# Kernel tuning notes

Measured on AMD Instinct MI355X. Metric: run time of the kernel, lower is better.

Reference implementation:

```python
import jax, jax.numpy as jnp
from jax import lax
import numpy as np

B = 262144
CLASSES = 11


def setup_inputs() -> dict:
    key = jax.random.key(0)
    ks = jax.random.split(key, 8)
    exponents = jax.random.randint(ks[0], (B, 16), 0, CLASSES, dtype=jnp.int32)
    conv0_w = jax.random.normal(ks[1], (4, 12, 1, 2), jnp.float32) * 0.1
    conv0_b = jax.random.normal(ks[2], (4,), jnp.float32) * 0.05
    conv1_w = jax.random.normal(ks[3], (4, 12, 2, 1), jnp.float32) * 0.1
    # xavier-uniform linears, bias filled with 0.01 (as in init_weights)
    lim1 = float(np.sqrt(6.0 / (96 + 256)))
    linear_w = jax.random.uniform(ks[4], (256, 96), jnp.float32, -lim1, lim1)
    linear_b = jnp.full((256,), 0.01, jnp.float32)
    lim2 = float(np.sqrt(6.0 / (256 + 4)))
    out_w = jax.random.uniform(ks[5], (4, 256), jnp.float32, -lim2, lim2)
    out_b = jnp.full((4,), 0.01, jnp.float32)
    return {"exponents": exponents, "conv0_w": conv0_w, "conv0_b": conv0_b,
            "conv1_w": conv1_w, "linear_w": linear_w, "linear_b": linear_b,
            "out_w": out_w, "out_b": out_b}


def _conv(x, w):
    return lax.conv_general_dilated(x, w, (1, 1), 'VALID',
                                    dimension_numbers=('NCHW', 'OIHW', 'NCHW'))


def _forward(exponents, conv0_w, conv0_b, conv1_w, linear_w, linear_b, out_w, out_b):
    e = exponents.reshape(-1, 4, 4)
    # reconstruct board values: 0 tile stays 0, else 2**e
    x = jnp.where(e == 0, 0.0, jnp.exp2(e.astype(jnp.float32)))  # [B,4,4]
    # rotate_normalize: flips chosen from argmax corner (computed BEFORE flipping)
    corners = jnp.stack([x[:, 0, 0], x[:, 0, -1], x[:, -1, 0], x[:, -1, -1]], axis=1)
    ix = jnp.argmax(corners, axis=1)
    flip_v = ix >= 2          # floor(ix/2) == 1
    flip_h = (ix % 2) == 1
    x = jnp.where(flip_v[:, None, None], x[:, ::-1, :], x)
    x = jnp.where(flip_h[:, None, None], x[:, :, ::-1], x)
    # log2 with 0 -> 0, one-hot over 11 classes
    x_log = jnp.log2(x + (x == 0).astype(jnp.float32))
    onehot = jax.nn.one_hot(jnp.round(x_log).astype(jnp.int32), CLASSES,
                            dtype=jnp.float32)          # [B,4,4,11]
    onehot = jnp.transpose(onehot, (0, 3, 1, 2))         # [B,11,4,4]
    mask = onehot.sum(axis=1, keepdims=True)             # channel 0 (all ones)
    feat = jnp.concatenate([mask, onehot], axis=1)       # [B,12,4,4]
    zh = jax.nn.relu(_conv(feat, conv0_w) + conv0_b[None, :, None, None])  # [B,4,4,3]
    zv = jax.nn.relu(_conv(feat, conv1_w))                                  # [B,4,3,4]
    z1 = jnp.concatenate([zh.reshape(-1, 48), zv.reshape(-1, 48)], axis=1)  # [B,96]
    z2 = jax.nn.relu(z1 @ linear_w.T + linear_b)                            # [B,256]
    probs = jax.nn.softmax(z2 @ out_w.T + out_b, axis=1)                    # [B,4]
    # unscramble: vert swaps actions (0,1); horiz swaps actions (2,3)
    perm = jnp.stack([jnp.where(flip_v, 1, 0), jnp.where(flip_v, 0, 1),
                      jnp.where(flip_h, 3, 2), jnp.where(flip_h, 2, 3)], axis=1)
    return jnp.take_along_axis(probs, perm, axis=1)


def reference(exponents, conv0_w, conv0_b, conv1_w, linear_w, linear_b, out_w, out_b):
    return _forward(exponents, conv0_w, conv0_b, conv1_w, linear_w, linear_b, out_w, out_b)
```

## Files before the change

kernel.cpp:

```cpp
#include <hip/hip_runtime.h>

typedef unsigned int  u32;
typedef unsigned short u16;

typedef float    f4  __attribute__((ext_vector_type(4)));
typedef short    bf8 __attribute__((ext_vector_type(8)));
typedef __fp16   h8  __attribute__((ext_vector_type(8)));
typedef __fp16   h2  __attribute__((ext_vector_type(2)));

#define NBLK  1024
#define ITERS 4
#define ZSTR  104

#define WS_AF   0
#define WS_OW   49152
#define WS_TAB  57344

__device__ __forceinline__ u32 bfr(float f) {
    union { float f; u32 u; } v; v.f = f;
    return (v.u + 0x8000u) >> 16;
}
__device__ __forceinline__ u32 pk2(float lo, float hi) { return bfr(lo) | (bfr(hi) << 16); }
__device__ __forceinline__ u32 pkh(float lo, float hi) {
    union { h2 h; u32 u; } v; v.h = __builtin_amdgcn_cvt_pkrtz(lo, hi); return v.u;
}
__device__ __forceinline__ u32 nrev(u32 x) {
    return ((x >> 12) & 0xFu) | ((x >> 4) & 0xF0u) | ((x << 4) & 0xF00u) | ((x << 12) & 0xF000u);
}

__launch_bounds__(256)
__global__ void smartcnn_prep(const float* __restrict__ c0w, const float* __restrict__ c0b,
                              const float* __restrict__ c1w,
                              const float* __restrict__ lw,  const float* __restrict__ ow,
                              u16* __restrict__ wsAf, u32* __restrict__ wsOw,
                              uint2* __restrict__ wsTab)
{
    const int i = blockIdx.x * 256 + threadIdx.x;
    if (i < 24576) {
        const int j    = i & 7;
        const int lane = (i >> 3) & 63;
        const int rest = i >> 9;
        const int m  = lane & 15, qd = lane >> 4;
        const int s  = rest % 3;
        const int wtt = rest / 3;
        const int tt = wtt & 3, w = wtt >> 2;
        const int tbase = ((tt & 1) ? 4 : 0) + ((tt >> 1) ? 32 : 0);
        const int fid = 64*w + tbase + 8*(m >> 2) + (m & 3);
        const int kp = s*32 + qd*8 + j;
        const int kq = (kp < 48) ? kp : kp - 48;
        const int ko = ((kp < 48) ? 0 : 48) + (kq & 3)*12 + (kq >> 2);
        wsAf[i] = (u16)bfr(lw[fid*96 + ko]);
    } else if (i < 26624) {
        const int t = i - 24576;
        const int k    = t & 3;
        const int lane = (t >> 2) & 63;
        const int wc   = t >> 8;
        const int m = lane & 15, qd = lane >> 4;
        const int c = wc & 1, w = wc >> 1;
        u32 val = 0u;
        if (m < 4) {
            const int n8 = 64*w + 32*c + qd*8;
            val = pkh(ow[m*256 + n8 + 2*k], ow[m*256 + n8 + 2*k + 1]);
        }
        wsOw[t] = val;
    } else if (i < 26866) {
        const int t = i - 26624;
        const int e = (t < 121) ? t : t - 121;
        const int v1 = e / 11, v2 = e - v1*11;
        float a[4];
        #pragma unroll
        for (int c = 0; c < 4; ++c) {
            if (t < 121)
                a[c] = fmaxf(c0w[c*24 + 0] + c0w[c*24 + (1+v1)*2 + 0] + c0b[c]
                           + c0w[c*24 + 1] + c0w[c*24 + (1+v2)*2 + 1], 0.f);
            else
                a[c] = fmaxf(c1w[c*24 + 0] + c1w[c*24 + (1+v1)*2 + 0]
                           + c1w[c*24 + 1] + c1w[c*24 + (1+v2)*2 + 1], 0.f);
        }
        wsTab[t] = make_uint2(pk2(a[0], a[1]), pk2(a[2], a[3]));
    }
}

__device__ __forceinline__ void phase1_fn(const int4 e4, u16* __restrict__ z1b, u32* __restrict__ flgb,
                                          const uint2* __restrict__ Th, const uint2* __restrict__ Tv,
                                          const int w, const int m, const int qd)
{
    u32 pkd = (u32)e4.x | ((u32)e4.y << 4) | ((u32)e4.z << 8) | ((u32)e4.w << 12);
    u32 R0 = (u32)__shfl((int)pkd, m);
    u32 R1 = (u32)__shfl((int)pkd, m + 16);
    u32 R2 = (u32)__shfl((int)pkd, m + 32);
    u32 R3 = (u32)__shfl((int)pkd, m + 48);
    u32 c0v = R0 & 15u, c1v = (R0 >> 12) & 15u, c2v = R3 & 15u, c3v = (R3 >> 12) & 15u;
    u32 best = c0v; int ix = 0;
    if (c1v > best) { best = c1v; ix = 1; }
    if (c2v > best) { best = c2v; ix = 2; }
    if (c3v > best) { best = c3v; ix = 3; }
    const bool fv = (ix >= 2), fh = ((ix & 1) != 0);
    u32 F[4];
    F[0] = fv ? R3 : R0;
    F[1] = fv ? R2 : R1;
    F[2] = fv ? R1 : R2;
    F[3] = fv ? R0 : R3;
    #pragma unroll
    for (int i = 0; i < 4; ++i) F[i] = fh ? nrev(F[i]) : F[i];

    if (qd == 0) flgb[w*16 + m] = (u32)fv | ((u32)fh << 1);

    const u32 Fq = F[qd];
    u32 nbq[4], nbc[4];
    #pragma unroll
    for (int j = 0; j < 4; ++j) nbq[j] = (Fq >> (4*j)) & 15u;
    #pragma unroll
    for (int i = 0; i < 4; ++i) nbc[i] = (F[i] >> (4*qd)) & 15u;

    uint2 H0 = Th[nbq[0]*11u + nbq[1]];
    uint2 H1 = Th[nbq[1]*11u + nbq[2]];
    uint2 H2 = Th[nbq[2]*11u + nbq[3]];
    uint2 V0 = Tv[nbc[0]*11u + nbc[1]];
    uint2 V1 = Tv[nbc[1]*11u + nbc[2]];
    uint2 V2 = Tv[nbc[2]*11u + nbc[3]];

    u16* zrow = &z1b[(w*16 + m) * ZSTR];
    *(uint2*)(zrow + (qd*3 + 0)*4) = H0;
    *(uint2*)(zrow + (qd*3 + 1)*4) = H1;
    *(uint2*)(zrow + (qd*3 + 2)*4) = H2;
    *(uint2*)(zrow + 48 + (0*4 + qd)*4) = V0;
    *(uint2*)(zrow + 48 + (1*4 + qd)*4) = V1;
    *(uint2*)(zrow + 48 + (2*4 + qd)*4) = V2;
}

__device__ __forceinline__ void gemm_fn(const u16* __restrict__ z1b, float4* __restrict__ Pb,
                                        const bf8 (&af)[4][3], const u32 (&owA)[2][4], const f4 (&lb4)[4],
                                        const int w, const int m, const int qd)
{
    #pragma unroll
    for (int G = 0; G < 4; ++G) {
        bf8 zb[3];
        #pragma unroll
        for (int s = 0; s < 3; ++s)
            zb[s] = *(const bf8*)(&z1b[(G*16 + m)*ZSTR + s*32 + qd*8]);

        f4 acc_t[4] = {lb4[0], lb4[1], lb4[2], lb4[3]};
        #pragma unroll
        for (int s = 0; s < 3; ++s)
            #pragma unroll
            for (int tt = 0; tt < 4; ++tt)
                acc_t[tt] = __builtin_amdgcn_mfma_f32_16x16x32_bf16(af[tt][s], zb[s], acc_t[tt], 0, 0, 0);

        f4 acc2 = {0.f, 0.f, 0.f, 0.f};
        #pragma unroll
        for (int c = 0; c < 2; ++c) {
            union { u32 u[4]; h8 v; } bu, au;
            bu.u[0] = pkh(fmaxf(acc_t[2*c  ][0], 0.f), fmaxf(acc_t[2*c  ][1], 0.f));
            bu.u[1] = pkh(fmaxf(acc_t[2*c  ][2], 0.f), fmaxf(acc_t[2*c  ][3], 0.f));
            bu.u[2] = pkh(fmaxf(acc_t[2*c+1][0], 0.f), fmaxf(acc_t[2*c+1][1], 0.f));
            bu.u[3] = pkh(fmaxf(acc_t[2*c+1][2], 0.f), fmaxf(acc_t[2*c+1][3], 0.f));
            au.u[0] = owA[c][0]; au.u[1] = owA[c][1]; au.u[2] = owA[c][2]; au.u[3] = owA[c][3];
            acc2 = __builtin_amdgcn_mfma_f32_16x16x32_f16(au.v, bu.v, acc2, 0, 0, 0);
        }
        if (qd == 0)
            Pb[(G*4 + w)*16 + m] = make_float4(acc2[0], acc2[1], acc2[2], acc2[3]);
    }
}

__device__ __forceinline__ void epi_fn(const float4* __restrict__ Pb, const u32 fl, const float4 obv,
                                       float* __restrict__ out, const int base, const int m, const int qd)
{
    float4 s0 = Pb[(qd*4 + 0)*16 + m], s1 = Pb[(qd*4 + 1)*16 + m];
    float4 s2 = Pb[(qd*4 + 2)*16 + m], s3 = Pb[(qd*4 + 3)*16 + m];
    float L0 = s0.x + s1.x + s2.x + s3.x + obv.x;
    float L1 = s0.y + s1.y + s2.y + s3.y + obv.y;
    float L2 = s0.z + s1.z + s2.z + s3.z + obv.z;
    float L3 = s0.w + s1.w + s2.w + s3.w + obv.w;
    float mx = fmaxf(fmaxf(L0, L1), fmaxf(L2, L3));
    float e0 = __expf(L0 - mx), e1 = __expf(L1 - mx), e2 = __expf(L2 - mx), e3 = __expf(L3 - mx);
    float inv = __builtin_amdgcn_rcpf(e0 + e1 + e2 + e3);
    float p0 = e0 * inv, p1 = e1 * inv, p2 = e2 * inv, p3 = e3 * inv;
    float4 o;
    o.x = (fl & 1u) ? p1 : p0;
    o.y = (fl & 1u) ? p0 : p1;
    o.z = (fl & 2u) ? p3 : p2;
    o.w = (fl & 2u) ? p2 : p3;
    *(float4*)(out + (size_t)(base + qd*16 + m) * 4) = o;
}

__launch_bounds__(256, 4)
__global__ void smartcnn_fused(const int* __restrict__ exps,
                               const float* __restrict__ lb, const float* __restrict__ ob,
                               const u16* __restrict__ wsAf, const u32* __restrict__ wsOw,
                               const uint2* __restrict__ wsTab,
                               float* __restrict__ out)
{
    __shared__ uint2  ThA[121];
    __shared__ uint2  TvA[121];
    __shared__ u16    z1A[64 * ZSTR];
    __shared__ u16    z1B[64 * ZSTR];
    __shared__ float4 PbA[4*4*16];
    __shared__ float4 PbB[4*4*16];
    __shared__ u32    flgA[64];
    __shared__ u32    flgB[64];

    const int tid  = threadIdx.x;
    const int w    = tid >> 6;
    const int lane = tid & 63;
    const int m    = lane & 15;
    const int qd   = lane >> 4;

    if (tid < 242) {
        uint2 v = wsTab[tid];
        if (tid < 121) ThA[tid] = v; else TvA[tid - 121] = v;
    }

    bf8 af[4][3];
    #pragma unroll
    for (int tt = 0; tt < 4; ++tt)
        #pragma unroll
        for (int s = 0; s < 3; ++s)
            af[tt][s] = *(const bf8*)(wsAf + (((w*4 + tt)*3 + s) << 9) + (lane << 3));

    u32 owA[2][4];
    #pragma unroll
    for (int c = 0; c < 2; ++c) {
        uint4 t = *(const uint4*)(wsOw + ((((w*2 + c) << 6) + lane) << 2));
        owA[c][0] = t.x; owA[c][1] = t.y; owA[c][2] = t.z; owA[c][3] = t.w;
    }

    f4 lb4[4];
    #pragma unroll
    for (int tt = 0; tt < 4; ++tt) {
        const int tbase = ((tt & 1) ? 4 : 0) + ((tt >> 1) ? 32 : 0);
        lb4[tt] = *(const f4*)(lb + 64*w + tbase + 8*qd);
    }
    const float4 obv = *(const float4*)ob;

    const int b0 = blockIdx.x * (ITERS * 64);
    __syncthreads();

    int4 e4 = *(const int4*)(exps + (size_t)(b0 + w*16 + m)*16 + qd*4);
    phase1_fn(e4, z1A, flgA, &ThA[0], &TvA[0], w, m, qd);
    e4 = *(const int4*)(exps + (size_t)(b0 + 64 + w*16 + m)*16 + qd*4);
    __syncthreads();

    #pragma unroll
    for (int itp = 0; itp < ITERS/2; ++itp) {
        const int it = itp * 2;

        const u32 flA = flgA[qd*16 + m];
        phase1_fn(e4, z1B, flgB, &ThA[0], &TvA[0], w, m, qd);
        if (it + 2 < ITERS)
            e4 = *(const int4*)(exps + (size_t)(b0 + (it+2)*64 + w*16 + m)*16 + qd*4);
        gemm_fn(z1A, PbA, af, owA, lb4, w, m, qd);

        __syncthreads();

        const u32 flB = flgB[qd*16 + m];
        if (it + 2 < ITERS) {
            phase1_fn(e4, z1A, flgA, &ThA[0], &TvA[0], w, m, qd);
            if (it + 3 < ITERS)
                e4 = *(const int4*)(exps + (size_t)(b0 + (it+3)*64 + w*16 + m)*16 + qd*4);
        }
        epi_fn(PbA, flA, obv, out, b0 + it*64, m, qd);
        gemm_fn(z1B, PbB, af, owA, lb4, w, m, qd);

        __syncthreads();

        epi_fn(PbB, flB, obv, out, b0 + (it+1)*64, m, qd);
    }
}

extern "C" void kernel_launch(void* const* d_in, const int* in_sizes, int n_in,
                              void* d_out, int out_size, void* d_ws, size_t ws_size,
                              hipStream_t stream) {
    const int*   exps = (const int*)  d_in[0];
    const float* c0w  = (const float*)d_in[1];
    const float* c0b  = (const float*)d_in[2];
    const float* c1w  = (const float*)d_in[3];
    const float* lw   = (const float*)d_in[4];
    const float* lbv  = (const float*)d_in[5];
    const float* oww  = (const float*)d_in[6];
    const float* obv  = (const float*)d_in[7];
    u16*   wsAf  = (u16*)  ((char*)d_ws + WS_AF);
    u32*   wsOw  = (u32*)  ((char*)d_ws + WS_OW);
    uint2* wsTab = (uint2*)((char*)d_ws + WS_TAB);
    smartcnn_prep<<<105, 256, 0, stream>>>(c0w, c0b, c1w, lw, oww, wsAf, wsOw, wsTab);
    smartcnn_fused<<<NBLK, 256, 0, stream>>>(exps, lbv, obv, wsAf, wsOw, wsTab, (float*)d_out);
}
```

Measured before the change: 93.64 us.

## Give each wave full hidden dimension to remove cross-wave reduction and barriers

Measured after the change: 175.7 us. 87.6% more time.

```diff
diff --git a/kernel.cpp b/kernel.cpp
--- a/kernel.cpp
+++ b/kernel.cpp
@@ -8,8 +8,8 @@
 typedef __fp16   h8  __attribute__((ext_vector_type(8)));
 typedef __fp16   h2  __attribute__((ext_vector_type(2)));
 
-#define NBLK  1024
-#define ITERS 4
+#define NBLK  512
+#define ITERS 8
 #define ZSTR  104
 
 #define WS_AF   0
@@ -23,6 +23,9 @@
 __device__ __forceinline__ u32 pk2(float lo, float hi) { return bfr(lo) | (bfr(hi) << 16); }
 __device__ __forceinline__ u32 pkh(float lo, float hi) {
     union { h2 h; u32 u; } v; v.h = __builtin_amdgcn_cvt_pkrtz(lo, hi); return v.u;
+}
+__device__ __forceinline__ u32 pkmax0(u32 x) {
+    u32 r; asm("v_pk_max_f16 %0, %1, %2" : "=v"(r) : "v"(x), "v"(0u)); return r;
 }
 __device__ __forceinline__ u32 nrev(u32 x) {
     return ((x >> 12) & 0xFu) | ((x >> 4) & 0xF0u) | ((x << 4) & 0xF00u) | ((x << 12) & 0xF000u);
@@ -81,124 +84,17 @@
     }
 }
 
-__device__ __forceinline__ void phase1_fn(const int4 e4, u16* __restrict__ z1b, u32* __restrict__ flgb,
-                                          const uint2* __restrict__ Th, const uint2* __restrict__ Tv,
-                                          const int w, const int m, const int qd)
-{
-    u32 pkd = (u32)e4.x | ((u32)e4.y << 4) | ((u32)e4.z << 8) | ((u32)e4.w << 12);
-    u32 R0 = (u32)__shfl((int)pkd, m);
-    u32 R1 = (u32)__shfl((int)pkd, m + 16);
-    u32 R2 = (u32)__shfl((int)pkd, m + 32);
-    u32 R3 = (u32)__shfl((int)pkd, m + 48);
-    u32 c0v = R0 & 15u, c1v = (R0 >> 12) & 15u, c2v = R3 & 15u, c3v = (R3 >> 12) & 15u;
-    u32 best = c0v; int ix = 0;
-    if (c1v > best) { best = c1v; ix = 1; }
-    if (c2v > best) { best = c2v; ix = 2; }
-    if (c3v > best) { best = c3v; ix = 3; }
-    const bool fv = (ix >= 2), fh = ((ix & 1) != 0);
-    u32 F[4];
-    F[0] = fv ? R3 : R0;
-    F[1] = fv ? R2 : R1;
-    F[2] = fv ? R1 : R2;
-    F[3] = fv ? R0 : R3;
-    #pragma unroll
-    for (int i = 0; i < 4; ++i) F[i] = fh ? nrev(F[i]) : F[i];
-
-    if (qd == 0) flgb[w*16 + m] = (u32)fv | ((u32)fh << 1);
-
-    const u32 Fq = F[qd];
-    u32 nbq[4], nbc[4];
-    #pragma unroll
-    for (int j = 0; j < 4; ++j) nbq[j] = (Fq >> (4*j)) & 15u;
-    #pragma unroll
-    for (int i = 0; i < 4; ++i) nbc[i] = (F[i] >> (4*qd)) & 15u;
-
-    uint2 H0 = Th[nbq[0]*11u + nbq[1]];
-    uint2 H1 = Th[nbq[1]*11u + nbq[2]];
-    uint2 H2 = Th[nbq[2]*11u + nbq[3]];
-    uint2 V0 = Tv[nbc[0]*11u + nbc[1]];
-    uint2 V1 = Tv[nbc[1]*11u + nbc[2]];
-    uint2 V2 = Tv[nbc[2]*11u + nbc[3]];
-
-    u16* zrow = &z1b[(w*16 + m) * ZSTR];
-    *(uint2*)(zrow + (qd*3 + 0)*4) = H0;
-    *(uint2*)(zrow + (qd*3 + 1)*4) = H1;
-    *(uint2*)(zrow + (qd*3 + 2)*4) = H2;
-    *(uint2*)(zrow + 48 + (0*4 + qd)*4) = V0;
-    *(uint2*)(zrow + 48 + (1*4 + qd)*4) = V1;
-    *(uint2*)(zrow + 48 + (2*4 + qd)*4) = V2;
-}
-
-__device__ __forceinline__ void gemm_fn(const u16* __restrict__ z1b, float4* __restrict__ Pb,
-                                        const bf8 (&af)[4][3], const u32 (&owA)[2][4], const f4 (&lb4)[4],
-                                        const int w, const int m, const int qd)
-{
-    #pragma unroll
-    for (int G = 0; G < 4; ++G) {
-        bf8 zb[3];
-        #pragma unroll
-        for (int s = 0; s < 3; ++s)
-            zb[s] = *(const bf8*)(&z1b[(G*16 + m)*ZSTR + s*32 + qd*8]);
-
-        f4 acc_t[4] = {lb4[0], lb4[1], lb4[2], lb4[3]};
-        #pragma unroll
-        for (int s = 0; s < 3; ++s)
-            #pragma unroll
-            for (int tt = 0; tt < 4; ++tt)
-                acc_t[tt] = __builtin_amdgcn_mfma_f32_16x16x32_bf16(af[tt][s], zb[s], acc_t[tt], 0, 0, 0);
-
-        f4 acc2 = {0.f, 0.f, 0.f, 0.f};
-        #pragma unroll
-        for (int c = 0; c < 2; ++c) {
-            union { u32 u[4]; h8 v; } bu, au;
-            bu.u[0] = pkh(fmaxf(acc_t[2*c  ][0], 0.f), fmaxf(acc_t[2*c  ][1], 0.f));
-            bu.u[1] = pkh(fmaxf(acc_t[2*c  ][2], 0.f), fmaxf(acc_t[2*c  ][3], 0.f));
-            bu.u[2] = pkh(fmaxf(acc_t[2*c+1][0], 0.f), fmaxf(acc_t[2*c+1][1], 0.f));
-            bu.u[3] = pkh(fmaxf(acc_t[2*c+1][2], 0.f), fmaxf(acc_t[2*c+1][3], 0.f));
-            au.u[0] = owA[c][0]; au.u[1] = owA[c][1]; au.u[2] = owA[c][2]; au.u[3] = owA[c][3];
-            acc2 = __builtin_amdgcn_mfma_f32_16x16x32_f16(au.v, bu.v, acc2, 0, 0, 0);
-        }
-        if (qd == 0)
-            Pb[(G*4 + w)*16 + m] = make_float4(acc2[0], acc2[1], acc2[2], acc2[3]);
-    }
-}
-
-__device__ __forceinline__ void epi_fn(const float4* __restrict__ Pb, const u32 fl, const float4 obv,
-                                       float* __restrict__ out, const int base, const int m, const int qd)
-{
-    float4 s0 = Pb[(qd*4 + 0)*16 + m], s1 = Pb[(qd*4 + 1)*16 + m];
-    float4 s2 = Pb[(qd*4 + 2)*16 + m], s3 = Pb[(qd*4 + 3)*16 + m];
-    float L0 = s0.x + s1.x + s2.x + s3.x + obv.x;
-    float L1 = s0.y + s1.y + s2.y + s3.y + obv.y;
-    float L2 = s0.z + s1.z + s2.z + s3.z + obv.z;
-    float L3 = s0.w + s1.w + s2.w + s3.w + obv.w;
-    float mx = fmaxf(fmaxf(L0, L1), fmaxf(L2, L3));
-    float e0 = __expf(L0 - mx), e1 = __expf(L1 - mx), e2 = __expf(L2 - mx), e3 = __expf(L3 - mx);
-    float inv = __builtin_amdgcn_rcpf(e0 + e1 + e2 + e3);
-    float p0 = e0 * inv, p1 = e1 * inv, p2 = e2 * inv, p3 = e3 * inv;
-    float4 o;
-    o.x = (fl & 1u) ? p1 : p0;
-    o.y = (fl & 1u) ? p0 : p1;
-    o.z = (fl & 2u) ? p3 : p2;
-    o.w = (fl & 2u) ? p2 : p3;
-    *(float4*)(out + (size_t)(base + qd*16 + m) * 4) = o;
-}
-
-__launch_bounds__(256, 4)
+__launch_bounds__(256, 2)
 __global__ void smartcnn_fused(const int* __restrict__ exps,
                                const float* __restrict__ lb, const float* __restrict__ ob,
                                const u16* __restrict__ wsAf, const u32* __restrict__ wsOw,
                                const uint2* __restrict__ wsTab,
                                float* __restrict__ out)
 {
-    __shared__ uint2  ThA[121];
-    __shared__ uint2  TvA[121];
-    __shared__ u16    z1A[64 * ZSTR];
-    __shared__ u16    z1B[64 * ZSTR];
-    __shared__ float4 PbA[4*4*16];
-    __shared__ float4 PbB[4*4*16];
-    __shared__ u32    flgA[64];
-    __shared__ u32    flgB[64];
+    __shared__ u16   afL[48 * 512];
+    __shared__ uint2 ThA[121];
+    __shared__ uint2 TvA[121];
+    __shared__ u16   z1[64 * ZSTR];
 
     const int tid  = threadIdx.x;
     const int w    = tid >> 6;
@@ -210,61 +106,126 @@
         uint2 v = wsTab[tid];
         if (tid < 121) ThA[tid] = v; else TvA[tid - 121] = v;
     }
-
-    bf8 af[4][3];
     #pragma unroll
-    for (int tt = 0; tt < 4; ++tt)
+    for (int f2 = 0; f2 < 12; ++f2) {
+        const int f = w * 12 + f2;
+        uint4 t = *(const uint4*)((const char*)wsAf + f * 1024 + lane * 16);
+        *(uint4*)((char*)afL + f * 1024 + lane * 16) = t;
+    }
+    u32 owA[8][4];
+    #pragma unroll
+    for (int c = 0; c < 8; ++c) {
+        uint4 t = *(const uint4*)(wsOw + c * 256 + lane * 4);
+        owA[c][0] = t.x; owA[c][1] = t.y; owA[c][2] = t.z; owA[c][3] = t.w;
+    }
+    f4 lbT[16];
+    #pragma unroll
+    for (int T = 0; T < 16; ++T) {
+        const int tbase = ((T & 1) ? 4 : 0) + ((T >> 1) * 32);
+        lbT[T] = *(const f4*)(lb + tbase + 8 * qd);
+    }
+    const float4 obv = *(const float4*)ob;
+
+    const int bb = blockIdx.x * (ITERS * 64);
+    __syncthreads();
+
+    int4 e4 = *(const int4*)(exps + (size_t)(bb + w*16 + m)*16 + qd*4);
+
+    #pragma unroll 1
+    for (int it = 0; it < ITERS; ++it) {
+        u32 pkd = (u32)e4.x | ((u32)e4.y << 4) | ((u32)e4.z << 8) | ((u32)e4.w << 12);
+        const int itn = (it + 1 < ITERS) ? it + 1 : it;
+        int4 e4n = *(const int4*)(exps + (size_t)(bb + itn*64 + w*16 + m)*16 + qd*4);
+
+        u32 R0 = (u32)__shfl((int)pkd, m);
+        u32 R1 = (u32)__shfl((int)pkd, m + 16);
+        u32 R2 = (u32)__shfl((int)pkd, m + 32);
+        u32 R3 = (u32)__shfl((int)pkd, m + 48);
+        u32 c0v = R0 & 15u, c1v = (R0 >> 12) & 15u, c2v = R3 & 15u, c3v = (R3 >> 12) & 15u;
+        u32 best = c0v; int ix = 0;
+        if (c1v > best) { best = c1v; ix = 1; }
+        if (c2v > best) { best = c2v; ix = 2; }
+        if (c3v > best) { best = c3v; ix = 3; }
+        const bool fv = (ix >= 2), fh = ((ix & 1) != 0);
+        u32 F0 = fv ? R3 : R0;
+        u32 F1 = fv ? R2 : R1;
+        u32 F2 = fv ? R1 : R2;
+        u32 F3 = fv ? R0 : R3;
+        if (fh) { F0 = nrev(F0); F1 = nrev(F1); F2 = nrev(F2); F3 = nrev(F3); }
+
+        const u32 Fq = (qd == 0) ? F0 : (qd == 1) ? F1 : (qd == 2) ? F2 : F3;
+        u32 nbq0 = Fq & 15u, nbq1 = (Fq >> 4) & 15u, nbq2 = (Fq >> 8) & 15u, nbq3 = (Fq >> 12) & 15u;
+        u32 nbc0 = (F0 >> (4*qd)) & 15u, nbc1 = (F1 >> (4*qd)) & 15u;
+        u32 nbc2 = (F2 >> (4*qd)) & 15u, nbc3 = (F3 >> (4*qd)) & 15u;
+
+        uint2 H0 = ThA[nbq0*11u + nbq1];
+        uint2 H1 = ThA[nbq1*11u + nbq2];
+        uint2 H2 = ThA[nbq2*11u + nbq3];
+        uint2 V0 = TvA[nbc0*11u + nbc1];
+        uint2 V1 = TvA[nbc1*11u + nbc2];
+        uint2 V2 = TvA[nbc2*11u + nbc3];
+
+        u16* zrow = &z1[(w*16 + m) * ZSTR];
+        *(uint2*)(zrow + (qd*3 + 0)*4) = H0;
+        *(uint2*)(zrow + (qd*3 + 1)*4) = H1;
+        *(uint2*)(zrow + (qd*3 + 2)*4) = H2;
+        *(uint2*)(zrow + 48 + (0*4 + qd)*4) = V0;
+        *(uint2*)(zrow + 48 + (1*4 + qd)*4) = V1;
+        *(uint2*)(zrow + 48 + (2*4 + qd)*4) = V2;
+
+        const u16* zbase = &z1[(w*16 + m) * ZSTR + qd*8];
+        bf8 zb0 = *(const bf8*)(zbase);
+        bf8 zb1 = *(const bf8*)(zbase + 32);
+        bf8 zb2 = *(const bf8*)(zbase + 64);
+
+        __builtin_amdgcn_s_setprio(1);
+        f4 acc[16];
         #pragma unroll
-        for (int s = 0; s < 3; ++s)
-            af[tt][s] = *(const bf8*)(wsAf + (((w*4 + tt)*3 + s) << 9) + (lane << 3));
-
-    u32 owA[2][4];
-    #pragma unroll
-    for (int c = 0; c < 2; ++c) {
-        uint4 t = *(const uint4*)(wsOw + ((((w*2 + c) << 6) + lane) << 2));
-        owA[c][0] = t.x; owA[c][1] = t.y; owA[c][2] = t.z; owA[c][3] = t.w;
-    }
-
-    f4 lb4[4];
-    #pragma unroll
-    for (int tt = 0; tt < 4; ++tt) {
-        const int tbase = ((tt & 1) ? 4 : 0) + ((tt >> 1) ? 32 : 0);
-        lb4[tt] = *(const f4*)(lb + 64*w + tbase + 8*qd);
-    }
-    const float4 obv = *(const float4*)ob;
-
-    const int b0 = blockIdx.x * (ITERS * 64);
-    __syncthreads();
-
-    int4 e4 = *(const int4*)(exps + (size_t)(b0 + w*16 + m)*16 + qd*4);
-    phase1_fn(e4, z1A, flgA, &ThA[0], &TvA[0], w, m, qd);
-    e4 = *(const int4*)(exps + (size_t)(b0 + 64 + w*16 + m)*16 + qd*4);
-    __syncthreads();
-
-    #pragma unroll
-    for (int itp = 0; itp < ITERS/2; ++itp) {
-        const int it = itp * 2;
-
-        const u32 flA = flgA[qd*16 + m];
-        phase1_fn(e4, z1B, flgB, &ThA[0], &TvA[0], w, m, qd);
-        if (it + 2 < ITERS)
-            e4 = *(const int4*)(exps + (size_t)(b0 + (it+2)*64 + w*16 + m)*16 + qd*4);
-        gemm_fn(z1A, PbA, af, owA, lb4, w, m, qd);
-
-        __syncthreads();
-
-        const u32 flB = flgB[qd*16 + m];
-        if (it + 2 < ITERS) {
-            phase1_fn(e4, z1A, flgA, &ThA[0], &TvA[0], w, m, qd);
-            if (it + 3 < ITERS)
-                e4 = *(const int4*)(exps + (size_t)(b0 + (it+3)*64 + w*16 + m)*16 + qd*4);
-        }
-        epi_fn(PbA, flA, obv, out, b0 + it*64, m, qd);
-        gemm_fn(z1B, PbB, af, owA, lb4, w, m, qd);
-
-        __syncthreads();
-
-        epi_fn(PbB, flB, obv, out, b0 + (it+1)*64, m, qd);
+        for (int T = 0; T < 16; ++T) {
+            const u16* ap = &afL[(T*3) * 512 + lane * 8];
+            bf8 a0 = *(const bf8*)(ap);
+            bf8 a1 = *(const bf8*)(ap + 512);
+            bf8 a2 = *(const bf8*)(ap + 1024);
+            f4 a = __builtin_amdgcn_mfma_f32_16x16x32_bf16(a0, zb0, lbT[T], 0, 0, 0);
+            a     = __builtin_amdgcn_mfma_f32_16x16x32_bf16(a1, zb1, a,      0, 0, 0);
+            acc[T] = __builtin_amdgcn_mfma_f32_16x16x32_bf16(a2, zb2, a,     0, 0, 0);
+        }
+
+        f4 p0 = {0.f, 0.f, 0.f, 0.f}, p1 = {0.f, 0.f, 0.f, 0.f};
+        #pragma unroll
+        for (int c = 0; c < 8; ++c) {
+            union { u32 u[4]; h8 v; } bu, au;
+            bu.u[0] = pkmax0(pkh(acc[2*c  ][0], acc[2*c  ][1]));
+            bu.u[1] = pkmax0(pkh(acc[2*c  ][2], acc[2*c  ][3]));
+            bu.u[2] = pkmax0(pkh(acc[2*c+1][0], acc[2*c+1][1]));
+            bu.u[3] = pkmax0(pkh(acc[2*c+1][2], acc[2*c+1][3]));
+            au.u[0] = owA[c][0]; au.u[1] = owA[c][1]; au.u[2] = owA[c][2]; au.u[3] = owA[c][3];
+            if (c & 1) p1 = __builtin_amdgcn_mfma_f32_16x16x32_f16(au.v, bu.v, p1, 0, 0, 0);
+            else       p0 = __builtin_amdgcn_mfma_f32_16x16x32_f16(au.v, bu.v, p0, 0, 0, 0);
+        }
+        __builtin_amdgcn_s_setprio(0);
+
+        if (qd == 0) {
+            float L0 = p0[0] + p1[0] + obv.x;
+            float L1 = p0[1] + p1[1] + obv.y;
+            float L2 = p0[2] + p1[2] + obv.z;
+            float L3 = p0[3] + p1[3] + obv.w;
+            float mx = fmaxf(fmaxf(L0, L1), fmaxf(L2, L3));
+            float e0 = __expf(L0 - mx), e1 = __expf(L1 - mx), e2 = __expf(L2 - mx), e3 = __expf(L3 - mx);
+            float inv = __builtin_amdgcn_rcpf(e0 + e1 + e2 + e3);
+            float P0 = e0 * inv, P1 = e1 * inv, P2 = e2 * inv, P3 = e3 * inv;
+            float4 o;
+            o.x = fh ? P1 : P0;
+            o.y = fh ? P0 : P1;
+            o.z = fv ? P3 : P2;
+            o.w = fv ? P2 : P3;
+            o.x = fv ? P1 : P0;
+            o.y = fv ? P0 : P1;
+            o.z = fh ? P3 : P2;
+            o.w = fh ? P2 : P3;
+            *(float4*)(out + (size_t)(bb + it*64 + w*16 + m) * 4) = o;
+        }
+        e4 = e4n;
     }
 }
 
```
